# Kernel tuning notes

Measured on AMD Instinct MI355X. Metric: run time of the kernel, lower is better.

## Reference

```python
import jax, jax.numpy as jnp
import numpy as np

N_HEADS = 16
ROPE_BASE = 10000.0


def setup_inputs() -> dict:
    key = jax.random.key(0)
    k1, k2, k3 = jax.random.split(key, 3)
    B, L, D = 2, 2048, 2048
    x = jax.random.normal(k1, (B, L, D), dtype=jnp.float32)
    w_qkv = jax.random.normal(k2, (D, 3 * D), dtype=jnp.float32) * (1.0 / np.sqrt(D))
    w_out = jax.random.normal(k3, (D, D), dtype=jnp.float32) * (1.0 / np.sqrt(D))
    return {"x": x, "w_qkv": w_qkv, "w_out": w_out}


def _rope_cos_sin(L, head_dim, dtype):
    # inv_freq over even dims, freqs duplicated across both halves (HF convention)
    inv_freq = 1.0 / (ROPE_BASE ** (jnp.arange(0, head_dim, 2, dtype=jnp.float32) / head_dim))
    freqs = jnp.arange(L, dtype=jnp.float32)[:, None] * inv_freq[None, :]  # [L, hd/2]
    emb = jnp.concatenate([freqs, freqs], axis=-1)  # [L, hd]
    return jnp.cos(emb).astype(dtype), jnp.sin(emb).astype(dtype)


def _rotate_half(t):
    h = t.shape[-1] // 2
    return jnp.concatenate([-t[..., h:], t[..., :h]], axis=-1)


def reference(x, w_qkv, w_out):
    B, L, D = x.shape
    H = N_HEADS
    hd = D // H
    qkv = x @ w_qkv  # [B, L, 3D]
    q, k, v = jnp.split(qkv, 3, axis=-1)

    def heads(t):  # [B, L, D] -> [B, H, L, hd]
        return t.reshape(B, L, H, hd).transpose(0, 2, 1, 3)

    q, k, v = heads(q), heads(k), heads(v)
    cos, sin = _rope_cos_sin(L, hd, x.dtype)  # [L, hd] broadcast over B,H
    q = q * cos + _rotate_half(q) * sin
    k = k * cos + _rotate_half(k) * sin
    # SDPA, no mask, no dropout (eval), not causal
    scale = 1.0 / np.sqrt(hd)
    scores = jnp.einsum('bhld,bhsd->bhls', q, k) * scale
    attn = jax.nn.softmax(scores, axis=-1)
    y = jnp.einsum('bhls,bhsd->bhld', attn, v)  # [B, H, L, hd]
    y = y.transpose(0, 2, 1, 3).reshape(B, L, D)
    return y @ w_out
```

## Files before the change

kernel.cpp:

```cpp
#include <hip/hip_runtime.h>

typedef __attribute__((ext_vector_type(8))) short bf16x8;
typedef __attribute__((ext_vector_type(8))) unsigned short u16x8;
typedef __attribute__((ext_vector_type(4))) float f32x4;
typedef __attribute__((ext_vector_type(4))) unsigned short u16x4;

#define BB 2
#define LL 2048
#define DD 2048
#define HH 16
#define HDIM 128
#define MM 4096
#define NQKV 6144

__device__ __forceinline__ unsigned short f2bf(float f) {
    unsigned int u = __builtin_bit_cast(unsigned int, f);
    u += 0x7FFFu + ((u >> 16) & 1u);
    return (unsigned short)(u >> 16);
}
__device__ __forceinline__ float bf2f(unsigned short h) {
    unsigned int u = ((unsigned int)h) << 16;
    return __builtin_bit_cast(float, u);
}

__device__ __forceinline__ void gload16(const unsigned short* g, unsigned short* l) {
    __builtin_amdgcn_global_load_lds((const __attribute__((address_space(1))) void*)g,
                                     (__attribute__((address_space(3))) void*)l, 16, 0, 0);
}

__global__ __launch_bounds__(256) void k_cvt_bf16(const float* __restrict__ in,
                                                  unsigned short* __restrict__ out,
                                                  int n4) {
    int i = blockIdx.x * 256 + threadIdx.x;
    if (i < n4) {
        float4 v = reinterpret_cast<const float4*>(in)[i];
        u16x4 o;
        o[0] = f2bf(v.x); o[1] = f2bf(v.y); o[2] = f2bf(v.z); o[3] = f2bf(v.w);
        reinterpret_cast<u16x4*>(out)[i] = o;
    }
}

__global__ __launch_bounds__(256) void k_cvt_T(const float* __restrict__ in,
                                               unsigned short* __restrict__ out,
                                               int K, int N) {
    __shared__ unsigned short t[64][72];
    int n0 = blockIdx.x * 64, k0 = blockIdx.y * 64;
    int tid = threadIdx.x;
    int tr = tid >> 4, tc = tid & 15;
    #pragma unroll
    for (int i = 0; i < 4; ++i) {
        int k = i * 16 + tr;
        float4 v = *reinterpret_cast<const float4*>(in + (size_t)(k0 + k) * N + n0 + tc * 4);
        t[tc * 4 + 0][k] = f2bf(v.x);
        t[tc * 4 + 1][k] = f2bf(v.y);
        t[tc * 4 + 2][k] = f2bf(v.z);
        t[tc * 4 + 3][k] = f2bf(v.w);
    }
    __syncthreads();
    #pragma unroll
    for (int i = 0; i < 4; ++i) {
        int n = i * 16 + tr;
        u16x4 o = *reinterpret_cast<u16x4*>(&t[n][tc * 4]);
        *reinterpret_cast<u16x4*>(out + (size_t)(n0 + n) * K + k0 + tc * 4) = o;
    }
}

__global__ __launch_bounds__(256) void k_transV(const unsigned short* __restrict__ in,
                                                unsigned short* __restrict__ out) {
    __shared__ unsigned short t[64][68];
    int l0 = blockIdx.x * 64, d0 = blockIdx.y * 64;
    int bh = blockIdx.z;
    const unsigned short* ib = in + (size_t)bh * LL * HDIM;
    unsigned short* ob = out + (size_t)bh * HDIM * LL;
    int tid = threadIdx.x;
    int tr = tid >> 4, tc = tid & 15;
    #pragma unroll
    for (int i = 0; i < 4; ++i) {
        int l = i * 16 + tr;
        u16x4 v = *reinterpret_cast<const u16x4*>(ib + (size_t)(l0 + l) * HDIM + d0 + tc * 4);
        t[tc * 4 + 0][l] = v[0];
        t[tc * 4 + 1][l] = v[1];
        t[tc * 4 + 2][l] = v[2];
        t[tc * 4 + 3][l] = v[3];
    }
    __syncthreads();
    #pragma unroll
    for (int i = 0; i < 4; ++i) {
        int d = i * 16 + tr;
        u16x4 o = *reinterpret_cast<u16x4*>(&t[d][tc * 4]);
        *reinterpret_cast<u16x4*>(ob + (size_t)(d0 + d) * LL + l0 + tc * 4) = o;
    }
}

__global__ __launch_bounds__(256) void k_rope_table(float* __restrict__ ct,
                                                    float* __restrict__ st) {
    int idx = blockIdx.x * 256 + threadIdx.x;
    if (idx >= LL * 64) return;
    int pos = idx >> 6, d = idx & 63;
    float freq = __expf(-(float)d * (9.210340371976184f / 64.0f));
    float ang = (float)pos * freq;
    ct[idx] = cosf(ang);
    st[idx] = sinf(ang);
}

__global__ __launch_bounds__(256) void k_rope_apply(unsigned short* __restrict__ Q,
                                                    unsigned short* __restrict__ K,
                                                    const float* __restrict__ ct,
                                                    const float* __restrict__ st) {
    int idx = blockIdx.x * 256 + threadIdx.x;
    int d = idx & 63;
    int pos = (idx >> 6) & (LL - 1);
    int bh = idx >> 17;
    size_t base = ((size_t)bh * LL + pos) * HDIM;
    float c = ct[pos * 64 + d], s = st[pos * 64 + d];
    float q0 = bf2f(Q[base + d]), q1 = bf2f(Q[base + d + 64]);
    Q[base + d]      = f2bf(q0 * c - q1 * s);
    Q[base + d + 64] = f2bf(q1 * c + q0 * s);
    float k0 = bf2f(K[base + d]), k1 = bf2f(K[base + d + 64]);
    K[base + d]      = f2bf(k0 * c - k1 * s);
    K[base + d + 64] = f2bf(k1 * c + k0 * s);
}

__global__ __launch_bounds__(512, 2) void k_gemm384(const unsigned short* __restrict__ A,
                                                    const unsigned short* __restrict__ Bt,
                                                    unsigned short* __restrict__ outQ,
                                                    unsigned short* __restrict__ outK,
                                                    unsigned short* __restrict__ outV) {
    __shared__ unsigned short sm[3 * 20480];
    const int Kn = DD;
    const int tid = threadIdx.x;
    const int lane = tid & 63, w = tid >> 6;
    const int wm = w >> 2, wn = w & 3;
    const int lrow = lane & 15, lgrp = lane >> 4;
    const int NT = Kn / 32;

    int orig = blockIdx.x;
    int tau = (orig & 7) * 32 + (orig >> 3);
    const int m0 = (tau & 15) * 256, n0 = (tau >> 4) * 384;

    const int srow = lane >> 2, scol = lane & 3;
    const int scolg = ((scol ^ ((srow >> 1) & 3)) * 8);
    const int fcol  = ((lgrp ^ ((lrow >> 1) & 3)) * 8);

    f32x4 acc[8][6] = {};

    auto stageA = [&](int t, int r) {
        unsigned short* dst = sm + (t % 3) * 20480 + (r * 128 + w * 16) * 32;
        gload16(A + (size_t)(m0 + r * 128 + w * 16 + srow) * Kn + t * 32 + scolg, dst);
    };
    auto stageB = [&](int t, int r) {
        unsigned short* dst = sm + (t % 3) * 20480 + 8192 + (r * 128 + w * 16) * 32;
        gload16(Bt + (size_t)(n0 + r * 128 + w * 16 + srow) * Kn + t * 32 + scolg, dst);
    };

    auto body = [&](int t, bool doStage) {
        unsigned short* bufA = sm + (t % 3) * 20480;
        unsigned short* bufB = bufA + 8192;
        bf16x8 af[8], bfr[2];
        #pragma unroll
        for (int f = 0; f < 8; ++f)
            af[f] = *reinterpret_cast<const bf16x8*>(bufA + (wm * 128 + f * 16 + lrow) * 32 + fcol);
        bfr[0] = *reinterpret_cast<const bf16x8*>(bufB + (wn * 96 + 0 * 16 + lrow) * 32 + fcol);
        bfr[1] = *reinterpret_cast<const bf16x8*>(bufB + (wn * 96 + 1 * 16 + lrow) * 32 + fcol);
        if (doStage) { stageA(t + 2, 0); stageA(t + 2, 1); }
        __builtin_amdgcn_s_barrier();
        __builtin_amdgcn_s_setprio(1);
        #pragma unroll
        for (int fm = 0; fm < 8; ++fm)
            #pragma unroll
            for (int j = 0; j < 2; ++j)
                acc[fm][j] = __builtin_amdgcn_mfma_f32_16x16x32_bf16(af[fm], bfr[j], acc[fm][j], 0, 0, 0);
        __builtin_amdgcn_s_setprio(0);
        bfr[0] = *reinterpret_cast<const bf16x8*>(bufB + (wn * 96 + 2 * 16 + lrow) * 32 + fcol);
        bfr[1] = *reinterpret_cast<const bf16x8*>(bufB + (wn * 96 + 3 * 16 + lrow) * 32 + fcol);
        if (doStage) { stageB(t + 2, 0); stageB(t + 2, 1); }
        __builtin_amdgcn_s_barrier();
        __builtin_amdgcn_s_setprio(1);
        #pragma unroll
        for (int fm = 0; fm < 8; ++fm)
            #pragma unroll
            for (int j = 0; j < 2; ++j)
                acc[fm][2 + j] = __builtin_amdgcn_mfma_f32_16x16x32_bf16(af[fm], bfr[j], acc[fm][2 + j], 0, 0, 0);
        __builtin_amdgcn_s_setprio(0);
        bfr[0] = *reinterpret_cast<const bf16x8*>(bufB + (wn * 96 + 4 * 16 + lrow) * 32 + fcol);
        bfr[1] = *reinterpret_cast<const bf16x8*>(bufB + (wn * 96 + 5 * 16 + lrow) * 32 + fcol);
        if (doStage) { stageB(t + 2, 2); }
        __builtin_amdgcn_s_barrier();
        __builtin_amdgcn_s_setprio(1);
        #pragma unroll
        for (int fm = 0; fm < 8; ++fm)
            #pragma unroll
            for (int j = 0; j < 2; ++j)
                acc[fm][4 + j] = __builtin_amdgcn_mfma_f32_16x16x32_bf16(af[fm], bfr[j], acc[fm][4 + j], 0, 0, 0);
        __builtin_amdgcn_s_setprio(0);
    };

    stageA(0, 0); stageA(0, 1); stageB(0, 0); stageB(0, 1); stageB(0, 2);
    stageA(1, 0); stageA(1, 1); stageB(1, 0); stageB(1, 1); stageB(1, 2);
    asm volatile("s_waitcnt vmcnt(5)" ::: "memory");
    __builtin_amdgcn_s_barrier();

    for (int t = 0; t < NT - 2; ++t) {
        body(t, true);
        asm volatile("s_waitcnt vmcnt(5)" ::: "memory");
        __builtin_amdgcn_s_barrier();
    }
    body(NT - 2, false);
    asm volatile("s_waitcnt vmcnt(0)" ::: "memory");
    __builtin_amdgcn_s_barrier();
    body(NT - 1, false);

    #pragma unroll
    for (int fm = 0; fm < 8; ++fm) {
        int mrow = m0 + wm * 128 + fm * 16 + lgrp * 4;
        #pragma unroll
        for (int fn = 0; fn < 6; ++fn) {
            int ncol = n0 + wn * 96 + fn * 16 + lrow;
            int which = ncol >> 11;
            int rr = ncol & (DD - 1);
            int h = rr >> 7, d = rr & (HDIM - 1);
            unsigned short* dst = (which == 0) ? outQ : ((which == 1) ? outK : outV);
            #pragma unroll
            for (int i = 0; i < 4; ++i) {
                int m = mrow + i;
                int b = m >> 11, pos = m & (LL - 1);
                dst[((size_t)(b * HH + h) * LL + pos) * HDIM + d] = f2bf(acc[fm][fn][i]);
            }
        }
    }
}

__global__ __launch_bounds__(256) void k_gemm8(const unsigned short* __restrict__ A,
                                               const unsigned short* __restrict__ Bt,
                                               int Nn, int Kn,
                                               float* __restrict__ outC) {
    __shared__ unsigned short sm[4 * 8192];
    const int tid = threadIdx.x;
    const int lane = tid & 63, w = tid >> 6;
    const int wm = w >> 1, wn = w & 1;
    const int lrow = lane & 15, lgrp = lane >> 4;
    const int m0 = blockIdx.y * 128, n0 = blockIdx.x * 128;
    const int NT = Kn / 32;

    const int srow = lane >> 2, scol = lane & 3;
    const int scolg = ((scol ^ ((srow >> 1) & 3)) * 8);
    const int fcol  = ((lgrp ^ ((lrow >> 1) & 3)) * 8);

    f32x4 acc[4][4] = {};

    auto stage = [&](int t) {
        const int kb = t * 32;
        unsigned short* buf = sm + (t & 3) * 8192;
        #pragma unroll
        for (int i = 0; i < 2; ++i) {
            int row = i * 64 + w * 16 + srow;
            gload16(A  + (size_t)(m0 + row) * Kn + kb + scolg, buf + i * 2048 + w * 512);
            gload16(Bt + (size_t)(n0 + row) * Kn + kb + scolg, buf + 4096 + i * 2048 + w * 512);
        }
    };

    auto tile_body = [&](int t, bool do_stage) {
        unsigned short* buf = sm + (t & 3) * 8192;
        bf16x8 af[4], bfr[4];
        #pragma unroll
        for (int f = 0; f < 4; ++f)
            af[f] = *reinterpret_cast<const bf16x8*>(buf + (wm * 64 + f * 16 + lrow) * 32 + fcol);
        #pragma unroll
        for (int f = 0; f < 4; ++f)
            bfr[f] = *reinterpret_cast<const bf16x8*>(buf + 4096 + (wn * 64 + f * 16 + lrow) * 32 + fcol);
        if (do_stage) stage(t + 3);
        __builtin_amdgcn_s_barrier();
        __builtin_amdgcn_s_setprio(1);
        #pragma unroll
        for (int fm = 0; fm < 4; ++fm)
            #pragma unroll
            for (int fn = 0; fn < 4; ++fn)
                acc[fm][fn] = __builtin_amdgcn_mfma_f32_16x16x32_bf16(af[fm], bfr[fn], acc[fm][fn], 0, 0, 0);
        __builtin_amdgcn_s_setprio(0);
    };

    stage(0); stage(1); stage(2);
    asm volatile("s_waitcnt vmcnt(8)" ::: "memory");
    __builtin_amdgcn_s_barrier();

    for (int t = 0; t < NT - 3; ++t) {
        tile_body(t, true);
        asm volatile("s_waitcnt vmcnt(8)" ::: "memory");
        __builtin_amdgcn_s_barrier();
    }
    tile_body(NT - 3, false);
    asm volatile("s_waitcnt vmcnt(4)" ::: "memory");
    __builtin_amdgcn_s_barrier();
    tile_body(NT - 2, false);
    asm volatile("s_waitcnt vmcnt(0)" ::: "memory");
    __builtin_amdgcn_s_barrier();
    tile_body(NT - 1, false);

    #pragma unroll
    for (int fm = 0; fm < 4; ++fm) {
        int mrow = m0 + wm * 64 + fm * 16 + lgrp * 4;
        #pragma unroll
        for (int fn = 0; fn < 4; ++fn) {
            int ncol = n0 + wn * 64 + fn * 16 + lrow;
            #pragma unroll
            for (int i = 0; i < 4; ++i)
                outC[(size_t)(mrow + i) * (size_t)Nn + ncol] = acc[fm][fn][i];
        }
    }
}

__global__ __launch_bounds__(256, 2) void k_attn(const unsigned short* __restrict__ Q,
                                                 const unsigned short* __restrict__ K,
                                                 const unsigned short* __restrict__ Vt,
                                                 unsigned short* __restrict__ Y) {
    __shared__ unsigned short Kl[64][136];
    __shared__ unsigned short VTl[128][72];
    __shared__ unsigned short Pl[128][72];
    int tid = threadIdx.x;
    int lane = tid & 63, w = tid >> 6;
    int lrow = lane & 15, lgrp = lane >> 4;
    int orig = blockIdx.x;
    int id = (orig & 7) * 64 + (orig >> 3);
    int bh = id >> 4, qt = id & 15;
    int b = bh >> 4, h = bh & 15;
    const unsigned short* Qb = Q  + (size_t)bh * LL * HDIM;
    const unsigned short* Kb = K  + (size_t)bh * LL * HDIM;
    const unsigned short* Vb = Vt + (size_t)bh * HDIM * LL;
    int q0 = qt * 128 + w * 32;

    bf16x8 qf[2][4];
    #pragma unroll
    for (int rm = 0; rm < 2; ++rm)
        #pragma unroll
        for (int kk = 0; kk < 4; ++kk)
            qf[rm][kk] = *reinterpret_cast<const bf16x8*>(
                Qb + (size_t)(q0 + rm * 16 + lrow) * HDIM + kk * 32 + lgrp * 8);

    f32x4 accO[2][8] = {};
    f32x4 accL[2] = {};
    bf16x8 ones;
    #pragma unroll
    for (int j = 0; j < 8; ++j) ones[j] = (short)0x3F80;
    const float scale = 0.08838834764831845f;

    u16x8 kr[4], vr[4];
    auto sload = [&](int kt) {
        #pragma unroll
        for (int i = 0; i < 4; ++i) {
            int c = i * 256 + tid;
            kr[i] = *reinterpret_cast<const u16x8*>(Kb + (size_t)(kt * 64 + (c >> 4)) * HDIM + (c & 15) * 8);
            vr[i] = *reinterpret_cast<const u16x8*>(Vb + (size_t)(c >> 3) * LL + kt * 64 + (c & 7) * 8);
        }
    };
    auto swrite = [&]() {
        #pragma unroll
        for (int i = 0; i < 4; ++i) {
            int c = i * 256 + tid;
            *reinterpret_cast<u16x8*>(&Kl[c >> 4][(c & 15) * 8]) = kr[i];
            *reinterpret_cast<u16x8*>(&VTl[c >> 3][(c & 7) * 8]) = vr[i];
        }
    };

    sload(0);
    swrite();
    __syncthreads();

    for (int kt = 0; kt < LL / 64; ++kt) {
        if (kt + 1 < LL / 64) sload(kt + 1);

        f32x4 s[2][4] = {};
        __builtin_amdgcn_s_setprio(1);
        #pragma unroll
        for (int kn = 0; kn < 4; ++kn) {
            #pragma unroll
            for (int kk = 0; kk < 4; ++kk) {
                bf16x8 kf = *reinterpret_cast<const bf16x8*>(&Kl[kn * 16 + lrow][kk * 32 + lgrp * 8]);
                #pragma unroll
                for (int rm = 0; rm < 2; ++rm)
                    s[rm][kn] = __builtin_amdgcn_mfma_f32_16x16x32_bf16(qf[rm][kk], kf, s[rm][kn], 0, 0, 0);
            }
        }
        __builtin_amdgcn_s_setprio(0);

        #pragma unroll
        for (int rm = 0; rm < 2; ++rm)
            #pragma unroll
            for (int kn = 0; kn < 4; ++kn)
                #pragma unroll
                for (int i = 0; i < 4; ++i) {
                    float p = __expf(s[rm][kn][i] * scale);
                    Pl[w * 32 + rm * 16 + lgrp * 4 + i][kn * 16 + lrow] = f2bf(p);
                }

        __builtin_amdgcn_s_setprio(1);
        #pragma unroll
        for (int ks = 0; ks < 2; ++ks) {
            bf16x8 pa[2];
            #pragma unroll
            for (int rm = 0; rm < 2; ++rm) {
                pa[rm] = *reinterpret_cast<const bf16x8*>(&Pl[w * 32 + rm * 16 + lrow][ks * 32 + lgrp * 8]);
                accL[rm] = __builtin_amdgcn_mfma_f32_16x16x32_bf16(pa[rm], ones, accL[rm], 0, 0, 0);
            }
            #pragma unroll
            for (int dn = 0; dn < 8; ++dn) {
                bf16x8 vf = *reinterpret_cast<const bf16x8*>(&VTl[dn * 16 + lrow][ks * 32 + lgrp * 8]);
                #pragma unroll
                for (int rm = 0; rm < 2; ++rm)
                    accO[rm][dn] = __builtin_amdgcn_mfma_f32_16x16x32_bf16(pa[rm], vf, accO[rm][dn], 0, 0, 0);
            }
        }
        __builtin_amdgcn_s_setprio(0);

        __syncthreads();
        if (kt + 1 < LL / 64) {
            swrite();
            __syncthreads();
        }
    }

    #pragma unroll
    for (int rm = 0; rm < 2; ++rm)
        #pragma unroll
        for (int i = 0; i < 4; ++i) {
            float inv = 1.0f / accL[rm][i];
            int pos = q0 + rm * 16 + lgrp * 4 + i;
            #pragma unroll
            for (int dn = 0; dn < 8; ++dn) {
                int d = dn * 16 + lrow;
                Y[((size_t)b * LL + pos) * DD + h * HDIM + d] = f2bf(accO[rm][dn][i] * inv);
            }
        }
}

extern "C" void kernel_launch(void* const* d_in, const int* in_sizes, int n_in,
                              void* d_out, int out_size, void* d_ws, size_t ws_size,
                              hipStream_t stream) {
    const float* x     = (const float*)d_in[0];
    const float* wqkv  = (const float*)d_in[1];
    const float* wout  = (const float*)d_in[2];
    float* out = (float*)d_out;

    char* ws = (char*)d_ws;
    size_t off = 0;
    auto take = [&](size_t bytes) { char* p = ws + off; off += (bytes + 255) & ~(size_t)255; return p; };
    unsigned short* xb    = (unsigned short*)take((size_t)MM * DD * 2);
    unsigned short* wqkvT = (unsigned short*)take((size_t)DD * NQKV * 2);
    unsigned short* woutT = (unsigned short*)take((size_t)DD * DD * 2);
    unsigned short* Qb    = (unsigned short*)take((size_t)BB * HH * LL * HDIM * 2);
    unsigned short* Kb    = (unsigned short*)take((size_t)BB * HH * LL * HDIM * 2);
    unsigned short* Vb    = (unsigned short*)take((size_t)BB * HH * LL * HDIM * 2);
    unsigned short* Yb    = (unsigned short*)take((size_t)MM * DD * 2);
    float* ct             = (float*)take((size_t)LL * 64 * 4);
    float* st             = (float*)take((size_t)LL * 64 * 4);
    if (off > ws_size) return;
    unsigned short* VtB = xb;

    k_cvt_bf16<<<(MM * DD / 4 + 255) / 256, 256, 0, stream>>>(x, xb, MM * DD / 4);
    k_cvt_T<<<dim3(NQKV / 64, DD / 64), 256, 0, stream>>>(wqkv, wqkvT, DD, NQKV);
    k_cvt_T<<<dim3(DD / 64, DD / 64), 256, 0, stream>>>(wout, woutT, DD, DD);
    k_rope_table<<<(LL * 64 + 255) / 256, 256, 0, stream>>>(ct, st);

    k_gemm384<<<256, 512, 0, stream>>>(xb, wqkvT, Qb, Kb, Vb);
    k_transV<<<dim3(LL / 64, HDIM / 64, BB * HH), 256, 0, stream>>>(Vb, VtB);
    k_rope_apply<<<(BB * HH * LL * 64) / 256, 256, 0, stream>>>(Qb, Kb, ct, st);
    k_attn<<<BB * HH * (LL / 128), 256, 0, stream>>>(Qb, Kb, VtB, Yb);
    k_gemm8<<<dim3(DD / 128, MM / 128), 256, 0, stream>>>(Yb, woutT, DD, DD, out);
}
```

Measured before the change: 269.4 us.

## Use 32x32 MFMA with register-resident P in attention and retile output GEMM

Attention now computes the transposed scores (K·Q) with 32x32x16 MFMAs so the probabilities come out in a register layout that can be packed to bf16 with v_cvt_pk and permlane32 swaps and fed straight into the PV MFMA. This removes the P round-trip through shared memory. K/V tiles are double-buffered in LDS so the second barrier per iteration goes away. The output projection GEMM becomes a 512-thread, 256x128-tile kernel on a 1D swizzled grid, which reuses each B tile across more rows but adds LDS and register pressure.

```diff
diff --git a/kernel.cpp b/kernel.cpp
--- a/kernel.cpp
+++ b/kernel.cpp
@@ -3,7 +3,10 @@
 typedef __attribute__((ext_vector_type(8))) short bf16x8;
 typedef __attribute__((ext_vector_type(8))) unsigned short u16x8;
 typedef __attribute__((ext_vector_type(4))) float f32x4;
+typedef __attribute__((ext_vector_type(16))) float f32x16;
 typedef __attribute__((ext_vector_type(4))) unsigned short u16x4;
+typedef __attribute__((ext_vector_type(4))) unsigned int u32x4;
+typedef unsigned int u32;
 
 #define BB 2
 #define LL 2048
@@ -26,6 +29,15 @@
 __device__ __forceinline__ void gload16(const unsigned short* g, unsigned short* l) {
     __builtin_amdgcn_global_load_lds((const __attribute__((address_space(1))) void*)g,
                                      (__attribute__((address_space(3))) void*)l, 16, 0, 0);
+}
+
+__device__ __forceinline__ u32 cvtpk(float lo, float hi) {
+    u32 r;
+    asm("v_cvt_pk_bf16_f32 %0, %1, %2" : "=v"(r) : "v"(lo), "v"(hi));
+    return r;
+}
+__device__ __forceinline__ void plswap(u32& a, u32& b) {
+    asm("v_permlane32_swap_b32 %0, %1" : "+v"(a), "+v"(b));
 }
 
 __global__ __launch_bounds__(256) void k_cvt_bf16(const float* __restrict__ in,
@@ -230,17 +242,20 @@
     }
 }
 
-__global__ __launch_bounds__(256) void k_gemm8(const unsigned short* __restrict__ A,
-                                               const unsigned short* __restrict__ Bt,
-                                               int Nn, int Kn,
-                                               float* __restrict__ outC) {
-    __shared__ unsigned short sm[4 * 8192];
+__global__ __launch_bounds__(512) void k_gemm2x(const unsigned short* __restrict__ A,
+                                                const unsigned short* __restrict__ Bt,
+                                                float* __restrict__ outC) {
+    __shared__ unsigned short sm[4 * 12288];
+    const int Kn = DD, Nn = DD;
     const int tid = threadIdx.x;
     const int lane = tid & 63, w = tid >> 6;
     const int wm = w >> 1, wn = w & 1;
     const int lrow = lane & 15, lgrp = lane >> 4;
-    const int m0 = blockIdx.y * 128, n0 = blockIdx.x * 128;
     const int NT = Kn / 32;
+
+    int orig = blockIdx.x;
+    int tau = (orig & 7) * 32 + (orig >> 3);
+    const int m0 = (tau & 15) * 256, n0 = (tau >> 4) * 128;
 
     const int srow = lane >> 2, scol = lane & 3;
     const int scolg = ((scol ^ ((srow >> 1) & 3)) * 8);
@@ -250,24 +265,21 @@
 
     auto stage = [&](int t) {
         const int kb = t * 32;
-        unsigned short* buf = sm + (t & 3) * 8192;
-        #pragma unroll
-        for (int i = 0; i < 2; ++i) {
-            int row = i * 64 + w * 16 + srow;
-            gload16(A  + (size_t)(m0 + row) * Kn + kb + scolg, buf + i * 2048 + w * 512);
-            gload16(Bt + (size_t)(n0 + row) * Kn + kb + scolg, buf + 4096 + i * 2048 + w * 512);
-        }
+        unsigned short* buf = sm + (t & 3) * 12288;
+        gload16(A  + (size_t)(m0 + w * 16 + srow) * Kn + kb + scolg,        buf + w * 512);
+        gload16(A  + (size_t)(m0 + 128 + w * 16 + srow) * Kn + kb + scolg,  buf + 4096 + w * 512);
+        gload16(Bt + (size_t)(n0 + w * 16 + srow) * Kn + kb + scolg,        buf + 8192 + w * 512);
     };
 
     auto tile_body = [&](int t, bool do_stage) {
-        unsigned short* buf = sm + (t & 3) * 8192;
+        unsigned short* buf = sm + (t & 3) * 12288;
         bf16x8 af[4], bfr[4];
         #pragma unroll
         for (int f = 0; f < 4; ++f)
             af[f] = *reinterpret_cast<const bf16x8*>(buf + (wm * 64 + f * 16 + lrow) * 32 + fcol);
         #pragma unroll
         for (int f = 0; f < 4; ++f)
-            bfr[f] = *reinterpret_cast<const bf16x8*>(buf + 4096 + (wn * 64 + f * 16 + lrow) * 32 + fcol);
+            bfr[f] = *reinterpret_cast<const bf16x8*>(buf + 8192 + (wn * 64 + f * 16 + lrow) * 32 + fcol);
         if (do_stage) stage(t + 3);
         __builtin_amdgcn_s_barrier();
         __builtin_amdgcn_s_setprio(1);
@@ -280,16 +292,16 @@
     };
 
     stage(0); stage(1); stage(2);
-    asm volatile("s_waitcnt vmcnt(8)" ::: "memory");
+    asm volatile("s_waitcnt vmcnt(6)" ::: "memory");
     __builtin_amdgcn_s_barrier();
 
     for (int t = 0; t < NT - 3; ++t) {
         tile_body(t, true);
-        asm volatile("s_waitcnt vmcnt(8)" ::: "memory");
+        asm volatile("s_waitcnt vmcnt(6)" ::: "memory");
         __builtin_amdgcn_s_barrier();
     }
     tile_body(NT - 3, false);
-    asm volatile("s_waitcnt vmcnt(4)" ::: "memory");
+    asm volatile("s_waitcnt vmcnt(3)" ::: "memory");
     __builtin_amdgcn_s_barrier();
     tile_body(NT - 2, false);
     asm volatile("s_waitcnt vmcnt(0)" ::: "memory");
@@ -313,31 +325,28 @@
                                                  const unsigned short* __restrict__ K,
                                                  const unsigned short* __restrict__ Vt,
                                                  unsigned short* __restrict__ Y) {
-    __shared__ unsigned short Kl[64][136];
-    __shared__ unsigned short VTl[128][72];
-    __shared__ unsigned short Pl[128][72];
+    __shared__ unsigned short Kl[2][64][136];
+    __shared__ unsigned short VTl[2][128][72];
     int tid = threadIdx.x;
     int lane = tid & 63, w = tid >> 6;
-    int lrow = lane & 15, lgrp = lane >> 4;
+    int l31 = lane & 31, hl = lane >> 5;
     int orig = blockIdx.x;
     int id = (orig & 7) * 64 + (orig >> 3);
     int bh = id >> 4, qt = id & 15;
-    int b = bh >> 4, h = bh & 15;
+    int b = bh >> 4, hh = bh & 15;
     const unsigned short* Qb = Q  + (size_t)bh * LL * HDIM;
     const unsigned short* Kb = K  + (size_t)bh * LL * HDIM;
     const unsigned short* Vb = Vt + (size_t)bh * HDIM * LL;
     int q0 = qt * 128 + w * 32;
 
-    bf16x8 qf[2][4];
-    #pragma unroll
-    for (int rm = 0; rm < 2; ++rm)
-        #pragma unroll
-        for (int kk = 0; kk < 4; ++kk)
-            qf[rm][kk] = *reinterpret_cast<const bf16x8*>(
-                Qb + (size_t)(q0 + rm * 16 + lrow) * HDIM + kk * 32 + lgrp * 8);
-
-    f32x4 accO[2][8] = {};
-    f32x4 accL[2] = {};
+    bf16x8 qf[8];
+    #pragma unroll
+    for (int kk = 0; kk < 8; ++kk)
+        qf[kk] = *reinterpret_cast<const bf16x8*>(
+            Qb + (size_t)(q0 + l31) * HDIM + kk * 16 + hl * 8);
+
+    f32x16 accO[4] = {};
+    f32x16 accL = {};
     bf16x8 ones;
     #pragma unroll
     for (int j = 0; j < 8; ++j) ones[j] = (short)0x3F80;
@@ -352,84 +361,84 @@
             vr[i] = *reinterpret_cast<const u16x8*>(Vb + (size_t)(c >> 3) * LL + kt * 64 + (c & 7) * 8);
         }
     };
-    auto swrite = [&]() {
+    auto swrite = [&](int buf) {
         #pragma unroll
         for (int i = 0; i < 4; ++i) {
             int c = i * 256 + tid;
-            *reinterpret_cast<u16x8*>(&Kl[c >> 4][(c & 15) * 8]) = kr[i];
-            *reinterpret_cast<u16x8*>(&VTl[c >> 3][(c & 7) * 8]) = vr[i];
+            *reinterpret_cast<u16x8*>(&Kl[buf][c >> 4][(c & 15) * 8]) = kr[i];
+            *reinterpret_cast<u16x8*>(&VTl[buf][c >> 3][(c & 7) * 8]) = vr[i];
         }
     };
 
     sload(0);
-    swrite();
+    swrite(0);
     __syncthreads();
 
     for (int kt = 0; kt < LL / 64; ++kt) {
+        int cb = kt & 1;
         if (kt + 1 < LL / 64) sload(kt + 1);
 
-        f32x4 s[2][4] = {};
-        __builtin_amdgcn_s_setprio(1);
-        #pragma unroll
-        for (int kn = 0; kn < 4; ++kn) {
-            #pragma unroll
-            for (int kk = 0; kk < 4; ++kk) {
-                bf16x8 kf = *reinterpret_cast<const bf16x8*>(&Kl[kn * 16 + lrow][kk * 32 + lgrp * 8]);
+        f32x16 s[2] = {};
+        __builtin_amdgcn_s_setprio(1);
+        #pragma unroll
+        for (int kk = 0; kk < 8; ++kk) {
+            bf16x8 kf0 = *reinterpret_cast<const bf16x8*>(&Kl[cb][l31][kk * 16 + hl * 8]);
+            bf16x8 kf1 = *reinterpret_cast<const bf16x8*>(&Kl[cb][32 + l31][kk * 16 + hl * 8]);
+            s[0] = __builtin_amdgcn_mfma_f32_32x32x16_bf16(kf0, qf[kk], s[0], 0, 0, 0);
+            s[1] = __builtin_amdgcn_mfma_f32_32x32x16_bf16(kf1, qf[kk], s[1], 0, 0, 0);
+        }
+        __builtin_amdgcn_s_setprio(0);
+
+        bf16x8 pa[2][2];
+        #pragma unroll
+        for (int kn = 0; kn < 2; ++kn) {
+            float p[16];
+            #pragma unroll
+            for (int r = 0; r < 16; ++r) p[r] = __expf(s[kn][r] * scale);
+            #pragma unroll
+            for (int ksub = 0; ksub < 2; ++ksub) {
+                const int bse = ksub * 8;
+                u32 a0 = cvtpk(p[bse + 0], p[bse + 1]);
+                u32 a1 = cvtpk(p[bse + 2], p[bse + 3]);
+                u32 b0 = cvtpk(p[bse + 4], p[bse + 5]);
+                u32 b1 = cvtpk(p[bse + 6], p[bse + 7]);
+                plswap(a0, b0);
+                plswap(a1, b1);
+                u32x4 fw; fw[0] = a0; fw[1] = a1; fw[2] = b0; fw[3] = b1;
+                pa[kn][ksub] = __builtin_bit_cast(bf16x8, fw);
+            }
+        }
+
+        __builtin_amdgcn_s_setprio(1);
+        #pragma unroll
+        for (int kn = 0; kn < 2; ++kn)
+            #pragma unroll
+            for (int ksub = 0; ksub < 2; ++ksub) {
+                accL = __builtin_amdgcn_mfma_f32_32x32x16_bf16(pa[kn][ksub], ones, accL, 0, 0, 0);
                 #pragma unroll
-                for (int rm = 0; rm < 2; ++rm)
-                    s[rm][kn] = __builtin_amdgcn_mfma_f32_16x16x32_bf16(qf[rm][kk], kf, s[rm][kn], 0, 0, 0);
+                for (int dn = 0; dn < 4; ++dn) {
+                    bf16x8 vf = *reinterpret_cast<const bf16x8*>(
+                        &VTl[cb][dn * 32 + l31][kn * 32 + ksub * 16 + hl * 8]);
+                    accO[dn] = __builtin_amdgcn_mfma_f32_32x32x16_bf16(pa[kn][ksub], vf, accO[dn], 0, 0, 0);
+                }
             }
-        }
-        __builtin_amdgcn_s_setprio(0);
-
-        #pragma unroll
-        for (int rm = 0; rm < 2; ++rm)
-            #pragma unroll
-            for (int kn = 0; kn < 4; ++kn)
-                #pragma unroll
-                for (int i = 0; i < 4; ++i) {
-                    float p = __expf(s[rm][kn][i] * scale);
-                    Pl[w * 32 + rm * 16 + lgrp * 4 + i][kn * 16 + lrow] = f2bf(p);
-                }
-
-        __builtin_amdgcn_s_setprio(1);
-        #pragma unroll
-        for (int ks = 0; ks < 2; ++ks) {
-            bf16x8 pa[2];
-            #pragma unroll
-            for (int rm = 0; rm < 2; ++rm) {
-                pa[rm] = *reinterpret_cast<const bf16x8*>(&Pl[w * 32 + rm * 16 + lrow][ks * 32 + lgrp * 8]);
-                accL[rm] = __builtin_amdgcn_mfma_f32_16x16x32_bf16(pa[rm], ones, accL[rm], 0, 0, 0);
-            }
-            #pragma unroll
-            for (int dn = 0; dn < 8; ++dn) {
-                bf16x8 vf = *reinterpret_cast<const bf16x8*>(&VTl[dn * 16 + lrow][ks * 32 + lgrp * 8]);
-                #pragma unroll
-                for (int rm = 0; rm < 2; ++rm)
-                    accO[rm][dn] = __builtin_amdgcn_mfma_f32_16x16x32_bf16(pa[rm], vf, accO[rm][dn], 0, 0, 0);
-            }
-        }
-        __builtin_amdgcn_s_setprio(0);
-
+        __builtin_amdgcn_s_setprio(0);
+
+        if (kt + 1 < LL / 64) swrite(cb ^ 1);
         __syncthreads();
-        if (kt + 1 < LL / 64) {
-            swrite();
-            __syncthreads();
-        }
-    }
-
-    #pragma unroll
-    for (int rm = 0; rm < 2; ++rm)
-        #pragma unroll
-        for (int i = 0; i < 4; ++i) {
-            float inv = 1.0f / accL[rm][i];
-            int pos = q0 + rm * 16 + lgrp * 4 + i;
-            #pragma unroll
-            for (int dn = 0; dn < 8; ++dn) {
-                int d = dn * 16 + lrow;
-                Y[((size_t)b * LL + pos) * DD + h * HDIM + d] = f2bf(accO[rm][dn][i] * inv);
-            }
-        }
+    }
+
+    #pragma unroll
+    for (int r = 0; r < 16; ++r) {
+        float inv = 1.0f / accL[r];
+        int qrow = (r & 3) + 8 * (r >> 2) + 4 * hl;
+        int pos = q0 + qrow;
+        #pragma unroll
+        for (int dn = 0; dn < 4; ++dn) {
+            int d = dn * 32 + l31;
+            Y[((size_t)b * LL + pos) * DD + hh * HDIM + d] = f2bf(accO[dn][r] * inv);
+        }
+    }
 }
 
 extern "C" void kernel_launch(void* const* d_in, const int* in_sizes, int n_in,
@@ -464,5 +473,5 @@
     k_transV<<<dim3(LL / 64, HDIM / 64, BB * HH), 256, 0, stream>>>(Vb, VtB);
     k_rope_apply<<<(BB * HH * LL * 64) / 256, 256, 0, stream>>>(Qb, Kb, ct, st);
     k_attn<<<BB * HH * (LL / 128), 256, 0, stream>>>(Qb, Kb, VtB, Yb);
-    k_gemm8<<<dim3(DD / 128, MM / 128), 256, 0, stream>>>(Yb, woutT, DD, DD, out);
-}
+    k_gemm2x<<<256, 512, 0, stream>>>(Yb, woutT, out);
+}
```

New measurement: 254.2 us. 5.7% less time.
